# Optimization experiments

Hardware: AMD Instinct MI355X
Metric: run time of the kernel (lower is better)

Reference implementation:

```python
import jax, jax.numpy as jnp
import numpy as np
import math

K, D_FEAT, L_FACT, N = 128, 512, 64, 4096


def setup_inputs() -> dict:
    key = jax.random.key(0)
    k1, k2, k3, k4 = jax.random.split(key, 4)
    x = jax.random.normal(k1, (N, D_FEAT), dtype=jnp.float32)
    MU = jax.random.normal(k2, (K, D_FEAT), dtype=jnp.float32)
    A = jax.random.normal(k3, (K, D_FEAT, L_FACT), dtype=jnp.float32) * 0.1
    D = jax.random.uniform(k4, (K, D_FEAT), dtype=jnp.float32, minval=0.5, maxval=1.5)
    PI = jnp.ones((K,), dtype=jnp.float32) / K
    return {"x": x, "MU": MU, "A": A, "D": D, "PI": PI}


def reference(x, MU, A, D, PI):
    # Woodbury-identity MFA log-likelihood: Sigma_k = A_k A_k^T + diag(D_k^2)
    Kc, d, l = A.shape
    iD = D ** -2.0                                    # (K, d)  inverse diagonal noise
    AiD = A * iD[:, :, None]                          # (K, d, l) = diag(iD) @ A
    # L_k = I_l + A_k^T diag(iD_k) A_k   (small l x l capacitance matrix)
    Lmat = jnp.eye(l, dtype=x.dtype)[None] + jnp.einsum('kdl,kdm->klm', A, AiD)
    iL = jnp.linalg.inv(Lmat)                         # (K, l, l)
    # q1[k,n] = sum_d iD[k,d] * (x[n,d] - MU[k,d])^2, expanded to avoid (K,N,d)
    q1 = ((x ** 2) @ iD.T                             # (N, K)
          - 2.0 * (x @ (iD * MU).T)
          + jnp.sum(iD * MU ** 2, axis=1)[None, :]).T  # (K, N)
    # t[k,n,:] = (diag(iD_k) A_k)^T (x_n - MU_k)
    t = jnp.einsum('nd,kdl->knl', x, AiD) - jnp.einsum('kd,kdl->kl', MU, AiD)[:, None, :]
    # q2[k,n] = t^T iL_k t  (Woodbury correction quadratic form)
    q2 = jnp.einsum('knl,klm,knm->kn', t, iL, t)      # (K, N)
    m_d = q1 - q2                                     # Mahalanobis distances (K, N)
    log_det_L = jnp.linalg.slogdet(Lmat)[1]           # L is PD -> log(det(L))
    log_det_Sigma = log_det_L - jnp.sum(jnp.log(iD), axis=1)
    const = d * math.log(2.0 * math.pi)
    # NOTE: original code adds PI (not log PI) -- kept faithful.
    per_comp = PI[:, None] - 0.5 * ((const + log_det_Sigma)[:, None] + m_d)  # (K, N)
    return jax.scipy.special.logsumexp(per_comp, axis=0)  # (N,)
```

## Files before the change

kernel.cpp:

```cpp
#include <hip/hip_runtime.h>
#include <math.h>


#define KC 128
#define DF 512
#define LF 64
#define NN 4096

typedef __attribute__((ext_vector_type(8))) short short8;
typedef __attribute__((ext_vector_type(4))) float f32x4;

static __device__ __forceinline__ unsigned short bfr(float f) {
  union { float f; unsigned u; } v; v.f = f;
  return (unsigned short)((v.u + 0x7FFFu + ((v.u >> 16) & 1u)) >> 16);
}
static __device__ __forceinline__ float b2f(unsigned short u) {
  union { unsigned u; float f; } v; v.u = ((unsigned)u) << 16; return v.f;
}
static __device__ __forceinline__ void ldst16(void* lds, const void* g) {
  __builtin_amdgcn_global_load_lds((const __attribute__((address_space(1))) void*)g,
                                   (__attribute__((address_space(3))) void*)lds,
                                   16, 0, 0);
}

__global__ __launch_bounds__(256) void mfa_prep(const float* __restrict__ x,
                                                const float* __restrict__ A,
                                                const float* __restrict__ Dp,
                                                unsigned short* __restrict__ xaug,
                                                unsigned short* __restrict__ As,
                                                unsigned short* __restrict__ Ast) {
  int b = blockIdx.x, tid = threadIdx.x;
  if (b < 1024) {
    int k = b >> 3, dc = b & 7;
    __shared__ float siDs[64];
    __shared__ unsigned short Tr[64][72];
    if (tid < 64) siDs[tid] = 1.0f / Dp[k * DF + dc * 64 + tid];
    __syncthreads();
#pragma unroll
    for (int q = 0; q < 4; ++q) {
      int f = q * 256 + tid;
      int dd = f >> 4, i4 = (f & 15) * 4;
      float4 v = *reinterpret_cast<const float4*>(&A[((size_t)(k * DF + dc * 64 + dd)) * LF + i4]);
      float s = siDs[dd];
      ushort4 u;
      u.x = bfr(v.x * s); u.y = bfr(v.y * s); u.z = bfr(v.z * s); u.w = bfr(v.w * s);
      *reinterpret_cast<ushort4*>(&As[((size_t)(k * DF + dc * 64 + dd)) * LF + i4]) = u;
      *reinterpret_cast<ushort4*>(&Tr[dd][i4]) = u;
    }
    __syncthreads();
    int i = tid >> 2, ds0 = (tid & 3) * 16;
    unsigned short t16[16];
#pragma unroll
    for (int e = 0; e < 16; ++e) t16[e] = Tr[ds0 + e][i];
    uint4 v0, v1;
    v0.x = (unsigned)t16[0] | ((unsigned)t16[1] << 16);
    v0.y = (unsigned)t16[2] | ((unsigned)t16[3] << 16);
    v0.z = (unsigned)t16[4] | ((unsigned)t16[5] << 16);
    v0.w = (unsigned)t16[6] | ((unsigned)t16[7] << 16);
    v1.x = (unsigned)t16[8] | ((unsigned)t16[9] << 16);
    v1.y = (unsigned)t16[10] | ((unsigned)t16[11] << 16);
    v1.z = (unsigned)t16[12] | ((unsigned)t16[13] << 16);
    v1.w = (unsigned)t16[14] | ((unsigned)t16[15] << 16);
    size_t ro = ((size_t)(k * LF + i)) * DF + dc * 64 + ds0;
    *reinterpret_cast<uint4*>(&Ast[ro]) = v0;
    *reinterpret_cast<uint4*>(&Ast[ro + 8]) = v1;
  } else {
    int f = (b - 1024) * 256 + tid;
    float4 v = reinterpret_cast<const float4*>(x)[f];
    int n = f >> 7, c4 = (f & 127) << 2;
    ushort4 a, s;
    a.x = bfr(v.x); a.y = bfr(v.y); a.z = bfr(v.z); a.w = bfr(v.w);
    s.x = bfr(v.x * v.x); s.y = bfr(v.y * v.y); s.z = bfr(v.z * v.z); s.w = bfr(v.w * v.w);
    *reinterpret_cast<ushort4*>(&xaug[(size_t)n * 1024 + c4]) = a;
    *reinterpret_cast<ushort4*>(&xaug[(size_t)n * 1024 + 512 + c4]) = s;
  }
}

__global__ __launch_bounds__(256) void mfa_percomp(const float* __restrict__ MU,
                                                   const float* __restrict__ Dp,
                                                   const float* __restrict__ PI,
                                                   const unsigned short* __restrict__ Ast,
                                                   const unsigned short* __restrict__ As,
                                                   unsigned short* __restrict__ Waug,
                                                   unsigned short* __restrict__ Gt,
                                                   float* __restrict__ hws,
                                                   float* __restrict__ c0g) {
  int k = blockIdx.x, tid = threadIdx.x, lane = tid & 63, w = tid >> 6;
  __shared__ float S[64 * 132];
  __shared__ unsigned short Tile[64 * 64];
  __shared__ float smuS[DF];
  __shared__ float m2part[256];
  __shared__ float m2S[64];
  __shared__ float invd_s[64];
  __shared__ float redq[80];
  __shared__ float c0a_s;

  for (int idx = tid; idx < 4096; idx += 256) {
    int r = idx >> 6, c = idx & 63;
    S[r * 132 + 64 + c] = (r == c) ? 1.f : 0.f;
  }

  {
    float slog = 0.f, smu2 = 0.f;
#pragma unroll
    for (int p = 0; p < 2; ++p) {
      int d = p * 256 + tid;
      float Dv = Dp[k * DF + d];
      float id = 1.f / (Dv * Dv);
      float mu = MU[k * DF + d];
      float wv = id * mu;
      smuS[d] = mu / Dv;
      Waug[(size_t)k * 1024 + d] = bfr(wv);
      Waug[(size_t)k * 1024 + 512 + d] = bfr(-0.5f * id);
      slog += logf(id);
      smu2 += wv * mu;
    }
#pragma unroll
    for (int m = 1; m < 64; m <<= 1) {
      slog += __shfl_xor(slog, m, 64);
      smu2 += __shfl_xor(smu2, m, 64);
    }
    if (lane == 0) { redq[w] = slog; redq[8 + w] = smu2; }
  }
  __syncthreads();
  if (tid == 0) {
    float sl = 0.f, sm = 0.f;
    for (int q = 0; q < 4; ++q) { sl += redq[q]; sm += redq[8 + q]; }
    c0a_s = PI[k] - 0.5f * (DF * 1.8378770664093453f + sm - sl);
  }

  f32x4 accL[4];
  f32x4 zero = {0.f, 0.f, 0.f, 0.f};
#pragma unroll
  for (int nj = 0; nj < 4; ++nj) accL[nj] = zero;
  int lr = lane >> 3, lc = lane & 7;
  int gcs = (lc ^ lr) * 8;
  float m2acc = 0.f;
  int mi_i = tid & 63, mi_g = tid >> 6;
  for (int kt = 0; kt < 8; ++kt) {
#pragma unroll
    for (int it = 0; it < 2; ++it) {
      int row = w * 8 + it * 32 + lr;
      ldst16(&Tile[(w * 8 + it * 32) * 64], Ast + ((size_t)(k * LF + row)) * DF + kt * 64 + gcs);
    }
    __syncthreads();
#pragma unroll
    for (int kk = 0; kk < 2; ++kk) {
      int sw = ((kk * 4 + (lane >> 4)) ^ (lane & 7)) * 8;
      short8 av = *reinterpret_cast<const short8*>(&Tile[(w * 16 + (lane & 15)) * 64 + sw]);
#pragma unroll
      for (int nj = 0; nj < 4; ++nj) {
        short8 bv = *reinterpret_cast<const short8*>(&Tile[(nj * 16 + (lane & 15)) * 64 + sw]);
        accL[nj] = __builtin_amdgcn_mfma_f32_16x16x32_bf16(av, bv, accL[nj], 0, 0, 0);
      }
    }
#pragma unroll
    for (int c2 = 0; c2 < 2; ++c2) {
      int g = mi_g * 2 + c2;
      int slot = g ^ (mi_i & 7);
      const unsigned* cp = reinterpret_cast<const unsigned*>(&Tile[mi_i * 64 + slot * 8]);
#pragma unroll
      for (int u2 = 0; u2 < 4; ++u2) {
        unsigned uu = cp[u2];
        int d0 = kt * 64 + g * 8 + u2 * 2;
        m2acc += b2f((unsigned short)(uu & 0xFFFF)) * smuS[d0];
        m2acc += b2f((unsigned short)(uu >> 16)) * smuS[d0 + 1];
      }
    }
    __syncthreads();
  }
#pragma unroll
  for (int nj = 0; nj < 4; ++nj)
#pragma unroll
    for (int reg = 0; reg < 4; ++reg) {
      int m = w * 16 + (lane >> 4) * 4 + reg;
      int n = nj * 16 + (lane & 15);
      S[m * 132 + n] = accL[nj][reg] + (m == n ? 1.f : 0.f);
    }
  m2part[tid] = m2acc;
  __syncthreads();
  if (tid < 64) m2S[tid] = m2part[tid] + m2part[tid + 64] + m2part[tid + 128] + m2part[tid + 192];

  {
    int rg = tid >> 4, cg = tid & 15;
    for (int Jo = 0; Jo < 16; ++Jo) {
      int J = Jo * 4;
      __syncthreads();
      f32x4 B0 = *reinterpret_cast<f32x4*>(&S[(J + 0) * 132 + J]);
      f32x4 B1 = *reinterpret_cast<f32x4*>(&S[(J + 1) * 132 + J]);
      f32x4 B2 = *reinterpret_cast<f32x4*>(&S[(J + 2) * 132 + J]);
      f32x4 B3 = *reinterpret_cast<f32x4*>(&S[(J + 3) * 132 + J]);
      int cc = J + 4 + cg * 4;
      f32x4 S0 = *reinterpret_cast<f32x4*>(&S[(J + 0) * 132 + cc]);
      f32x4 S1 = *reinterpret_cast<f32x4*>(&S[(J + 1) * 132 + cc]);
      f32x4 S2 = *reinterpret_cast<f32x4*>(&S[(J + 2) * 132 + cc]);
      f32x4 S3 = *reinterpret_cast<f32x4*>(&S[(J + 3) * 132 + cc]);
      f32x4 V[4], TGT[4];
#pragma unroll
      for (int a = 0; a < 4; ++a) {
        int r = J + rg + 16 * a;
        if (r < 64) {
          V[a] = *reinterpret_cast<f32x4*>(&S[r * 132 + J]);
          TGT[a] = *reinterpret_cast<f32x4*>(&S[r * 132 + cc]);
        }
      }
      __syncthreads();
      float p0 = 1.0f / B0[0];
      float m10 = B1[0] * p0;  B1 -= m10 * B0;
      float m20 = B2[0] * p0;  B2 -= m20 * B0;
      float m30 = B3[0] * p0;  B3 -= m30 * B0;
      float p1 = 1.0f / B1[1];
      float m21 = B2[1] * p1;  B2 -= m21 * B1;
      float m31 = B3[1] * p1;  B3 -= m31 * B1;
      float p2 = 1.0f / B2[2];
      float m32 = B3[2] * p2;  B3 -= m32 * B2;
      float p3 = 1.0f / B3[3];
      float T1_0 = -m10;
      float T2_1 = -m21, T2_0 = -m20 - m21 * T1_0;
      float T3_2 = -m32, T3_1 = -m31 - m32 * T2_1, T3_0 = -m30 - m31 * T1_0 - m32 * T2_0;
      if (cg == 0 && rg < 4) {
        f32x4 bw = (rg == 0) ? B0 : (rg == 1) ? B1 : (rg == 2) ? B2 : B3;
        *reinterpret_cast<f32x4*>(&S[(J + rg) * 132 + J]) = bw;
      }
#pragma unroll
      for (int a = 0; a < 4; ++a) {
        int r = J + rg + 16 * a;
        if (r < 64) {
          f32x4 v = V[a];
          float n0 = v[0] * p0;
          float t1 = v[1] - n0 * B0[1];
          float n1 = t1 * p1;
          float t2 = v[2] - n0 * B0[2] - n1 * B1[2];
          float n2 = t2 * p2;
          float t3 = v[3] - n0 * B0[3] - n1 * B1[3] - n2 * B2[3];
          float n3 = t3 * p3;
          int pi = r - J;
          if (pi < 1) n0 = 0.f;
          if (pi < 2) n1 = 0.f;
          if (pi < 3) n2 = 0.f;
          if (pi < 4) n3 = 0.f;
          float cA = n0 + n1 * T1_0 + n2 * T2_0 + n3 * T3_0;
          float cB = n1 + n2 * T2_1 + n3 * T3_1;
          float cC = n2 + n3 * T3_2;
          float cD = n3;
          f32x4 res = TGT[a] - cA * S0 - cB * S1 - cC * S2 - cD * S3;
          *reinterpret_cast<f32x4*>(&S[r * 132 + cc]) = res;
        }
      }
    }
  }
  __syncthreads();
  if (tid < 64) {
    float dg2 = S[tid * 132 + tid];
    invd_s[tid] = rsqrtf(dg2);
    redq[tid] = logf(dg2);
  }
  __syncthreads();
  if (tid == 0) {
    float s = 0.f;
    for (int q = 0; q < 64; ++q) s += redq[q];
    c0g[k] = c0a_s - 0.5f * s;
  }
  if (tid < 64) {
    float hsum = 0.f;
#pragma unroll
    for (int j2 = 0; j2 < 64; ++j2) hsum += S[tid * 132 + 64 + j2] * m2S[j2];
    hws[k * 64 + tid] = hsum * invd_s[tid];
  }
  unsigned short* Wbs = Tile;
  {
    int l = tid >> 2;
#pragma unroll
    for (int q = 0; q < 2; ++q) {
      int sc = (tid & 3) * 2 + q;
      int gch = sc ^ (l & 7);
      float il = invd_s[l];
      unsigned short t8[8];
#pragma unroll
      for (int e = 0; e < 8; ++e) t8[e] = bfr(il * S[l * 132 + 64 + gch * 8 + e]);
      uint4 val;
      val.x = (unsigned)t8[0] | ((unsigned)t8[1] << 16);
      val.y = (unsigned)t8[2] | ((unsigned)t8[3] << 16);
      val.z = (unsigned)t8[4] | ((unsigned)t8[5] << 16);
      val.w = (unsigned)t8[6] | ((unsigned)t8[7] << 16);
      *reinterpret_cast<uint4*>(&Wbs[l * 64 + sc * 8]) = val;
    }
  }
  __syncthreads();
  unsigned short* DsA = reinterpret_cast<unsigned short*>(S);
  unsigned short* CoutA = reinterpret_cast<unsigned short*>(S) + 8192;
  for (int dq = 0; dq < 4; ++dq) {
#pragma unroll
    for (int it = 0; it < 4; ++it) {
      int row = w * 8 + it * 32 + lr;
      ldst16(&DsA[(w * 8 + it * 32) * 64], As + ((size_t)(k * DF + dq * 128 + row)) * LF + gcs);
    }
    __syncthreads();
    f32x4 gacc[4][2];
#pragma unroll
    for (int mi = 0; mi < 4; ++mi)
#pragma unroll
      for (int nj = 0; nj < 2; ++nj) gacc[mi][nj] = zero;
#pragma unroll
    for (int kk = 0; kk < 2; ++kk) {
      int sw = ((kk * 4 + (lane >> 4)) ^ (lane & 7)) * 8;
      short8 av[4], bv[2];
#pragma unroll
      for (int mi = 0; mi < 4; ++mi)
        av[mi] = *reinterpret_cast<const short8*>(&Wbs[(mi * 16 + (lane & 15)) * 64 + sw]);
#pragma unroll
      for (int nj = 0; nj < 2; ++nj)
        bv[nj] = *reinterpret_cast<const short8*>(&DsA[(w * 32 + nj * 16 + (lane & 15)) * 64 + sw]);
#pragma unroll
      for (int mi = 0; mi < 4; ++mi)
#pragma unroll
        for (int nj = 0; nj < 2; ++nj)
          gacc[mi][nj] = __builtin_amdgcn_mfma_f32_16x16x32_bf16(av[mi], bv[nj], gacc[mi][nj], 0, 0, 0);
    }
    float siD[2];
#pragma unroll
    for (int nj = 0; nj < 2; ++nj)
      siD[nj] = 1.0f / Dp[k * DF + dq * 128 + w * 32 + nj * 16 + (lane & 15)];
#pragma unroll
    for (int mi = 0; mi < 4; ++mi)
#pragma unroll
      for (int nj = 0; nj < 2; ++nj) {
        int dl = w * 32 + nj * 16 + (lane & 15);
#pragma unroll
        for (int reg = 0; reg < 4; ++reg) {
          int l = mi * 16 + (lane >> 4) * 4 + reg;
          CoutA[l * 132 + dl] = bfr(gacc[mi][nj][reg] * siD[nj]);
        }
      }
    __syncthreads();
    {
      int l = tid >> 2, seg = (tid & 3) * 32;
      uint4* dst = reinterpret_cast<uint4*>(&Gt[((size_t)(k * LF + l)) * DF + dq * 128 + seg]);
#pragma unroll
      for (int u = 0; u < 4; ++u) {
        unsigned short t8[8];
#pragma unroll
        for (int e = 0; e < 8; ++e) t8[e] = CoutA[l * 132 + seg + u * 8 + e];
        uint4 val;
        val.x = (unsigned)t8[0] | ((unsigned)t8[1] << 16);
        val.y = (unsigned)t8[2] | ((unsigned)t8[3] << 16);
        val.z = (unsigned)t8[4] | ((unsigned)t8[5] << 16);
        val.w = (unsigned)t8[6] | ((unsigned)t8[7] << 16);
        dst[u] = val;
      }
    }
    __syncthreads();
  }
}

__global__ __launch_bounds__(256) void mfa_q1g(const unsigned short* __restrict__ xaug,
                                               const unsigned short* __restrict__ Waug,
                                               float* __restrict__ r12p) {
  int nb = blockIdx.x * 128, kq = blockIdx.y;
  int tid = threadIdx.x, lane = tid & 63, w = tid >> 6, wx = w & 1, wy = w >> 1;
  __shared__ unsigned short As[128 * 64];
  __shared__ unsigned short Bs[128 * 64];
  f32x4 acc[4][4];
  f32x4 zero = {0.f, 0.f, 0.f, 0.f};
#pragma unroll
  for (int mi = 0; mi < 4; ++mi)
#pragma unroll
    for (int nj = 0; nj < 4; ++nj) acc[mi][nj] = zero;
  const unsigned short* xg = xaug + (size_t)nb * 1024;
  int lr = lane >> 3, lc = lane & 7;
  int gcs = (lc ^ lr) * 8;
  for (int kt = 0; kt < 4; ++kt) {
    int kof = kq * 256 + kt * 64;
#pragma unroll
    for (int it = 0; it < 4; ++it) {
      int row = w * 8 + it * 32 + lr;
      ldst16(&As[(w * 8 + it * 32) * 64], xg + (size_t)row * 1024 + kof + gcs);
      ldst16(&Bs[(w * 8 + it * 32) * 64], Waug + (size_t)row * 1024 + kof + gcs);
    }
    __syncthreads();
#pragma unroll
    for (int kk = 0; kk < 2; ++kk) {
      int sw = ((kk * 4 + (lane >> 4)) ^ (lane & 7)) * 8;
      short8 av[4], bv[4];
#pragma unroll
      for (int mi = 0; mi < 4; ++mi)
        av[mi] = *reinterpret_cast<const short8*>(&As[(wy * 64 + mi * 16 + (lane & 15)) * 64 + sw]);
#pragma unroll
      for (int nj = 0; nj < 4; ++nj)
        bv[nj] = *reinterpret_cast<const short8*>(&Bs[(wx * 64 + nj * 16 + (lane & 15)) * 64 + sw]);
#pragma unroll
      for (int mi = 0; mi < 4; ++mi)
#pragma unroll
        for (int nj = 0; nj < 4; ++nj)
          acc[mi][nj] = __builtin_amdgcn_mfma_f32_16x16x32_bf16(av[mi], bv[nj], acc[mi][nj], 0, 0, 0);
    }
    __syncthreads();
  }
  float* outp = r12p + (size_t)kq * KC * NN;
#pragma unroll
  for (int mi = 0; mi < 4; ++mi)
#pragma unroll
    for (int nj = 0; nj < 4; ++nj) {
      int ccol = wx * 64 + nj * 16 + (lane & 15);
      int nrow = nb + wy * 64 + mi * 16 + (lane >> 4) * 4;
      float4 o;
      o.x = acc[mi][nj][0]; o.y = acc[mi][nj][1]; o.z = acc[mi][nj][2]; o.w = acc[mi][nj][3];
      *reinterpret_cast<float4*>(&outp[(size_t)ccol * NN + nrow]) = o;
    }
}

__global__ __launch_bounds__(256) void mfa_main(const unsigned short* __restrict__ xaug,
                                                const unsigned short* __restrict__ Gt,
                                                const float* __restrict__ hws,
                                                const float* __restrict__ c0g,
                                                const float* __restrict__ r12p,
                                                float* __restrict__ s2b) {
  int bx = blockIdx.x, by = blockIdx.y;
  int tid = threadIdx.x, lane = tid & 63, w = tid >> 6, wx = w & 1, wy = w >> 1;
  __shared__ unsigned short As[128 * 64];
  __shared__ unsigned short Bs[128 * 64];
  f32x4 acc[4][4];
  f32x4 zero = {0.f, 0.f, 0.f, 0.f};
#pragma unroll
  for (int mi = 0; mi < 4; ++mi)
#pragma unroll
    for (int nj = 0; nj < 4; ++nj) acc[mi][nj] = zero;
  int nbase = by * 128, cbase = bx * 128;
  const unsigned short* xg = xaug + (size_t)nbase * 1024;
  const unsigned short* gg = Gt + (size_t)cbase * DF;
  int lr = lane >> 3, lc = lane & 7;
  int gcs = (lc ^ lr) * 8;
  for (int kt = 0; kt < 8; ++kt) {
#pragma unroll
    for (int it = 0; it < 4; ++it) {
      int row = w * 8 + it * 32 + lr;
      ldst16(&As[(w * 8 + it * 32) * 64], xg + (size_t)row * 1024 + kt * 64 + gcs);
      ldst16(&Bs[(w * 8 + it * 32) * 64], gg + (size_t)row * DF + kt * 64 + gcs);
    }
    __syncthreads();
#pragma unroll
    for (int kk = 0; kk < 2; ++kk) {
      int sw = ((kk * 4 + (lane >> 4)) ^ (lane & 7)) * 8;
      short8 av[4], bv[4];
#pragma unroll
      for (int mi = 0; mi < 4; ++mi)
        av[mi] = *reinterpret_cast<const short8*>(&As[(wy * 64 + mi * 16 + (lane & 15)) * 64 + sw]);
#pragma unroll
      for (int nj = 0; nj < 4; ++nj)
        bv[nj] = *reinterpret_cast<const short8*>(&Bs[(wx * 64 + nj * 16 + (lane & 15)) * 64 + sw]);
#pragma unroll
      for (int mi = 0; mi < 4; ++mi)
#pragma unroll
        for (int nj = 0; nj < 4; ++nj)
          acc[mi][nj] = __builtin_amdgcn_mfma_f32_16x16x32_bf16(av[mi], bv[nj], acc[mi][nj], 0, 0, 0);
    }
    __syncthreads();
  }
  int comp = bx * 2 + wx;
  float hv[4];
#pragma unroll
  for (int nj = 0; nj < 4; ++nj) hv[nj] = hws[comp * 64 + nj * 16 + (lane & 15)];
  float cc = c0g[comp];
  int rbase = nbase + wy * 64;
#pragma unroll
  for (int mi = 0; mi < 4; ++mi) {
    f32x4 sv;
#pragma unroll
    for (int reg = 0; reg < 4; ++reg) {
      float s = 0.f;
#pragma unroll
      for (int nj = 0; nj < 4; ++nj) {
        float dlt = acc[mi][nj][reg] - hv[nj];
        s += dlt * dlt;
      }
      s += __shfl_xor(s, 1, 64);
      s += __shfl_xor(s, 2, 64);
      s += __shfl_xor(s, 4, 64);
      s += __shfl_xor(s, 8, 64);
      sv[reg] = s;
    }
    if ((lane & 15) == 0) {
      int nr = rbase + mi * 16 + (lane >> 4) * 4;
      size_t idx = (size_t)comp * NN + nr;
      float4 r0 = *reinterpret_cast<const float4*>(&r12p[idx]);
      float4 r1 = *reinterpret_cast<const float4*>(&r12p[(size_t)KC * NN + idx]);
      float4 r2 = *reinterpret_cast<const float4*>(&r12p[(size_t)2 * KC * NN + idx]);
      float4 r3 = *reinterpret_cast<const float4*>(&r12p[(size_t)3 * KC * NN + idx]);
      float4 o;
      o.x = 0.5f * sv[0] + cc + r0.x + r1.x + r2.x + r3.x;
      o.y = 0.5f * sv[1] + cc + r0.y + r1.y + r2.y + r3.y;
      o.z = 0.5f * sv[2] + cc + r0.z + r1.z + r2.z + r3.z;
      o.w = 0.5f * sv[3] + cc + r0.w + r1.w + r2.w + r3.w;
      *reinterpret_cast<float4*>(&s2b[idx]) = o;
    }
  }
}

__global__ __launch_bounds__(64) void mfa_lse(const float* __restrict__ s2b,
                                              float* __restrict__ out) {
  int n = blockIdx.x * 64 + threadIdx.x;
  float m = -3.0e38f, s = 0.f;
#pragma unroll 8
  for (int k = 0; k < KC; ++k) {
    float t = s2b[(size_t)k * NN + n];
    float nm = fmaxf(m, t);
    s = s * expf(m - nm) + expf(t - nm);
    m = nm;
  }
  out[n] = m + logf(s);
}

extern "C" void kernel_launch(void* const* d_in, const int* in_sizes, int n_in,
                              void* d_out, int out_size, void* d_ws, size_t ws_size,
                              hipStream_t stream) {
  const float* x  = (const float*)d_in[0];
  const float* MU = (const float*)d_in[1];
  const float* A  = (const float*)d_in[2];
  const float* Dp = (const float*)d_in[3];
  const float* PI = (const float*)d_in[4];
  float* out = (float*)d_out;

  char* base = (char*)d_ws;
  size_t off = 0;
  auto alloc = [&](size_t bytes) -> void* {
    void* p = base + off;
    off += (bytes + 255) & ~(size_t)255;
    return p;
  };
  unsigned short* xaug = (unsigned short*)alloc((size_t)NN * 1024 * 2);
  unsigned short* As   = (unsigned short*)alloc((size_t)KC * DF * LF * 2);
  unsigned short* Ast  = (unsigned short*)alloc((size_t)KC * LF * DF * 2);
  unsigned short* Waug = (unsigned short*)alloc((size_t)KC * 1024 * 2);
  unsigned short* Gt   = (unsigned short*)alloc((size_t)KC * LF * DF * 2);
  float* hws           = (float*)alloc((size_t)KC * 64 * 4);
  float* c0g           = (float*)alloc((size_t)KC * 4);
  float* r12p          = (float*)alloc((size_t)4 * KC * NN * 4);
  float* s2b           = (float*)alloc((size_t)KC * NN * 4);

  mfa_prep<<<3072, 256, 0, stream>>>(x, A, Dp, xaug, As, Ast);
  mfa_percomp<<<KC, 256, 0, stream>>>(MU, Dp, PI, Ast, As, Waug, Gt, hws, c0g);
  mfa_q1g<<<dim3(NN / 128, 4), 256, 0, stream>>>(xaug, Waug, r12p);
  mfa_main<<<dim3(64, NN / 128), 256, 0, stream>>>(xaug, Gt, hws, c0g, r12p, s2b);
  mfa_lse<<<NN / 64, 64, 0, stream>>>(s2b, out);
}
```

Before: 168.7 us.

## Fuse q1 GEMM into main kernel as extra heavy block column; batch percomp tile loads

Removes the separate mfa_q1g launch. mfa_main gets one extra block column (bx==0) that computes the full q1 GEMM over K=1024 against Waug and writes a single r12 buffer, which mfa_lse then adds. This replaces the four split-K partial buffers that mfa_main used to read. Separately, mfa_percomp now loads four Ast k-tiles per sync into the S shared buffer, cutting the number of barriers, and moves the identity initialisation to after the loop. The heavy column does twice the K-loop work of the other columns, which risks load imbalance and a long tail.

New measurement: 186.4 us. +10.5%, slower.

```diff
diff --git a/kernel.cpp b/kernel.cpp
--- a/kernel.cpp
+++ b/kernel.cpp
@@ -87,18 +87,14 @@
                                                    float* __restrict__ c0g) {
   int k = blockIdx.x, tid = threadIdx.x, lane = tid & 63, w = tid >> 6;
   __shared__ float S[64 * 132];
-  __shared__ unsigned short Tile[64 * 64];
+  __shared__ unsigned short Wbs[64 * 64];
   __shared__ float smuS[DF];
   __shared__ float m2part[256];
   __shared__ float m2S[64];
   __shared__ float invd_s[64];
   __shared__ float redq[80];
   __shared__ float c0a_s;
-
-  for (int idx = tid; idx < 4096; idx += 256) {
-    int r = idx >> 6, c = idx & 63;
-    S[r * 132 + 64 + c] = (r == c) ? 1.f : 0.f;
-  }
+  unsigned short* Tile = reinterpret_cast<unsigned short*>(S);
 
   {
     float slog = 0.f, smu2 = 0.f;
@@ -137,37 +133,50 @@
   int gcs = (lc ^ lr) * 8;
   float m2acc = 0.f;
   int mi_i = tid & 63, mi_g = tid >> 6;
-  for (int kt = 0; kt < 8; ++kt) {
-#pragma unroll
-    for (int it = 0; it < 2; ++it) {
-      int row = w * 8 + it * 32 + lr;
-      ldst16(&Tile[(w * 8 + it * 32) * 64], Ast + ((size_t)(k * LF + row)) * DF + kt * 64 + gcs);
-    }
-    __syncthreads();
-#pragma unroll
-    for (int kk = 0; kk < 2; ++kk) {
-      int sw = ((kk * 4 + (lane >> 4)) ^ (lane & 7)) * 8;
-      short8 av = *reinterpret_cast<const short8*>(&Tile[(w * 16 + (lane & 15)) * 64 + sw]);
-#pragma unroll
-      for (int nj = 0; nj < 4; ++nj) {
-        short8 bv = *reinterpret_cast<const short8*>(&Tile[(nj * 16 + (lane & 15)) * 64 + sw]);
-        accL[nj] = __builtin_amdgcn_mfma_f32_16x16x32_bf16(av, bv, accL[nj], 0, 0, 0);
-      }
-    }
-#pragma unroll
-    for (int c2 = 0; c2 < 2; ++c2) {
-      int g = mi_g * 2 + c2;
-      int slot = g ^ (mi_i & 7);
-      const unsigned* cp = reinterpret_cast<const unsigned*>(&Tile[mi_i * 64 + slot * 8]);
-#pragma unroll
-      for (int u2 = 0; u2 < 4; ++u2) {
-        unsigned uu = cp[u2];
-        int d0 = kt * 64 + g * 8 + u2 * 2;
-        m2acc += b2f((unsigned short)(uu & 0xFFFF)) * smuS[d0];
-        m2acc += b2f((unsigned short)(uu >> 16)) * smuS[d0 + 1];
-      }
-    }
-    __syncthreads();
+  for (int half = 0; half < 2; ++half) {
+    __syncthreads();
+#pragma unroll
+    for (int kt2 = 0; kt2 < 4; ++kt2) {
+      int kt = half * 4 + kt2;
+#pragma unroll
+      for (int it = 0; it < 2; ++it) {
+        int row = w * 8 + it * 32 + lr;
+        ldst16(&Tile[(kt2 * 64 + w * 8 + it * 32) * 64],
+               Ast + ((size_t)(k * LF + row)) * DF + kt * 64 + gcs);
+      }
+    }
+    __syncthreads();
+#pragma unroll
+    for (int kt2 = 0; kt2 < 4; ++kt2) {
+#pragma unroll
+      for (int kk = 0; kk < 2; ++kk) {
+        int sw = ((kk * 4 + (lane >> 4)) ^ (lane & 7)) * 8;
+        short8 av = *reinterpret_cast<const short8*>(&Tile[(kt2 * 64 + w * 16 + (lane & 15)) * 64 + sw]);
+#pragma unroll
+        for (int nj = 0; nj < 4; ++nj) {
+          short8 bv = *reinterpret_cast<const short8*>(&Tile[(kt2 * 64 + nj * 16 + (lane & 15)) * 64 + sw]);
+          accL[nj] = __builtin_amdgcn_mfma_f32_16x16x32_bf16(av, bv, accL[nj], 0, 0, 0);
+        }
+      }
+#pragma unroll
+      for (int c2 = 0; c2 < 2; ++c2) {
+        int g = mi_g * 2 + c2;
+        int slot = g ^ (mi_i & 7);
+        const unsigned* cp = reinterpret_cast<const unsigned*>(&Tile[(kt2 * 64 + mi_i) * 64 + slot * 8]);
+#pragma unroll
+        for (int u2 = 0; u2 < 4; ++u2) {
+          unsigned uu = cp[u2];
+          int d0 = (half * 4 + kt2) * 64 + g * 8 + u2 * 2;
+          m2acc += b2f((unsigned short)(uu & 0xFFFF)) * smuS[d0];
+          m2acc += b2f((unsigned short)(uu >> 16)) * smuS[d0 + 1];
+        }
+      }
+    }
+  }
+  __syncthreads();
+  for (int idx = tid; idx < 4096; idx += 256) {
+    int r = idx >> 6, c = idx & 63;
+    S[r * 132 + 64 + c] = (r == c) ? 1.f : 0.f;
   }
 #pragma unroll
   for (int nj = 0; nj < 4; ++nj)
@@ -267,7 +276,6 @@
     for (int j2 = 0; j2 < 64; ++j2) hsum += S[tid * 132 + 64 + j2] * m2S[j2];
     hws[k * 64 + tid] = hsum * invd_s[tid];
   }
-  unsigned short* Wbs = Tile;
   {
     int l = tid >> 2;
 #pragma unroll
@@ -289,6 +297,7 @@
   __syncthreads();
   unsigned short* DsA = reinterpret_cast<unsigned short*>(S);
   unsigned short* CoutA = reinterpret_cast<unsigned short*>(S) + 8192;
+  f32x4 zero2 = {0.f, 0.f, 0.f, 0.f};
   for (int dq = 0; dq < 4; ++dq) {
 #pragma unroll
     for (int it = 0; it < 4; ++it) {
@@ -300,7 +309,7 @@
 #pragma unroll
     for (int mi = 0; mi < 4; ++mi)
 #pragma unroll
-      for (int nj = 0; nj < 2; ++nj) gacc[mi][nj] = zero;
+      for (int nj = 0; nj < 2; ++nj) gacc[mi][nj] = zero2;
 #pragma unroll
     for (int kk = 0; kk < 2; ++kk) {
       int sw = ((kk * 4 + (lane >> 4)) ^ (lane & 7)) * 8;
@@ -353,67 +362,12 @@
   }
 }
 
-__global__ __launch_bounds__(256) void mfa_q1g(const unsigned short* __restrict__ xaug,
-                                               const unsigned short* __restrict__ Waug,
-                                               float* __restrict__ r12p) {
-  int nb = blockIdx.x * 128, kq = blockIdx.y;
-  int tid = threadIdx.x, lane = tid & 63, w = tid >> 6, wx = w & 1, wy = w >> 1;
-  __shared__ unsigned short As[128 * 64];
-  __shared__ unsigned short Bs[128 * 64];
-  f32x4 acc[4][4];
-  f32x4 zero = {0.f, 0.f, 0.f, 0.f};
-#pragma unroll
-  for (int mi = 0; mi < 4; ++mi)
-#pragma unroll
-    for (int nj = 0; nj < 4; ++nj) acc[mi][nj] = zero;
-  const unsigned short* xg = xaug + (size_t)nb * 1024;
-  int lr = lane >> 3, lc = lane & 7;
-  int gcs = (lc ^ lr) * 8;
-  for (int kt = 0; kt < 4; ++kt) {
-    int kof = kq * 256 + kt * 64;
-#pragma unroll
-    for (int it = 0; it < 4; ++it) {
-      int row = w * 8 + it * 32 + lr;
-      ldst16(&As[(w * 8 + it * 32) * 64], xg + (size_t)row * 1024 + kof + gcs);
-      ldst16(&Bs[(w * 8 + it * 32) * 64], Waug + (size_t)row * 1024 + kof + gcs);
-    }
-    __syncthreads();
-#pragma unroll
-    for (int kk = 0; kk < 2; ++kk) {
-      int sw = ((kk * 4 + (lane >> 4)) ^ (lane & 7)) * 8;
-      short8 av[4], bv[4];
-#pragma unroll
-      for (int mi = 0; mi < 4; ++mi)
-        av[mi] = *reinterpret_cast<const short8*>(&As[(wy * 64 + mi * 16 + (lane & 15)) * 64 + sw]);
-#pragma unroll
-      for (int nj = 0; nj < 4; ++nj)
-        bv[nj] = *reinterpret_cast<const short8*>(&Bs[(wx * 64 + nj * 16 + (lane & 15)) * 64 + sw]);
-#pragma unroll
-      for (int mi = 0; mi < 4; ++mi)
-#pragma unroll
-        for (int nj = 0; nj < 4; ++nj)
-          acc[mi][nj] = __builtin_amdgcn_mfma_f32_16x16x32_bf16(av[mi], bv[nj], acc[mi][nj], 0, 0, 0);
-    }
-    __syncthreads();
-  }
-  float* outp = r12p + (size_t)kq * KC * NN;
-#pragma unroll
-  for (int mi = 0; mi < 4; ++mi)
-#pragma unroll
-    for (int nj = 0; nj < 4; ++nj) {
-      int ccol = wx * 64 + nj * 16 + (lane & 15);
-      int nrow = nb + wy * 64 + mi * 16 + (lane >> 4) * 4;
-      float4 o;
-      o.x = acc[mi][nj][0]; o.y = acc[mi][nj][1]; o.z = acc[mi][nj][2]; o.w = acc[mi][nj][3];
-      *reinterpret_cast<float4*>(&outp[(size_t)ccol * NN + nrow]) = o;
-    }
-}
-
 __global__ __launch_bounds__(256) void mfa_main(const unsigned short* __restrict__ xaug,
                                                 const unsigned short* __restrict__ Gt,
+                                                const unsigned short* __restrict__ Waug,
                                                 const float* __restrict__ hws,
                                                 const float* __restrict__ c0g,
-                                                const float* __restrict__ r12p,
+                                                float* __restrict__ r12,
                                                 float* __restrict__ s2b) {
   int bx = blockIdx.x, by = blockIdx.y;
   int tid = threadIdx.x, lane = tid & 63, w = tid >> 6, wx = w & 1, wy = w >> 1;
@@ -425,17 +379,22 @@
   for (int mi = 0; mi < 4; ++mi)
 #pragma unroll
     for (int nj = 0; nj < 4; ++nj) acc[mi][nj] = zero;
-  int nbase = by * 128, cbase = bx * 128;
+  bool heavy = (bx == 0);
+  int nkt = heavy ? 16 : 8;
+  int nbase = by * 128;
   const unsigned short* xg = xaug + (size_t)nbase * 1024;
-  const unsigned short* gg = Gt + (size_t)cbase * DF;
+  const unsigned short* gg;
+  size_t bstride;
+  if (heavy) { gg = Waug; bstride = 1024; }
+  else       { gg = Gt + (size_t)((bx - 1) * 128) * DF; bstride = DF; }
   int lr = lane >> 3, lc = lane & 7;
   int gcs = (lc ^ lr) * 8;
-  for (int kt = 0; kt < 8; ++kt) {
+  for (int kt = 0; kt < nkt; ++kt) {
 #pragma unroll
     for (int it = 0; it < 4; ++it) {
       int row = w * 8 + it * 32 + lr;
       ldst16(&As[(w * 8 + it * 32) * 64], xg + (size_t)row * 1024 + kt * 64 + gcs);
-      ldst16(&Bs[(w * 8 + it * 32) * 64], gg + (size_t)row * DF + kt * 64 + gcs);
+      ldst16(&Bs[(w * 8 + it * 32) * 64], gg + (size_t)row * bstride + kt * 64 + gcs);
     }
     __syncthreads();
 #pragma unroll
@@ -456,53 +415,63 @@
     }
     __syncthreads();
   }
-  int comp = bx * 2 + wx;
-  float hv[4];
-#pragma unroll
-  for (int nj = 0; nj < 4; ++nj) hv[nj] = hws[comp * 64 + nj * 16 + (lane & 15)];
-  float cc = c0g[comp];
-  int rbase = nbase + wy * 64;
-#pragma unroll
-  for (int mi = 0; mi < 4; ++mi) {
-    f32x4 sv;
-#pragma unroll
-    for (int reg = 0; reg < 4; ++reg) {
-      float s = 0.f;
+  if (heavy) {
+#pragma unroll
+    for (int mi = 0; mi < 4; ++mi)
 #pragma unroll
       for (int nj = 0; nj < 4; ++nj) {
-        float dlt = acc[mi][nj][reg] - hv[nj];
-        s += dlt * dlt;
-      }
-      s += __shfl_xor(s, 1, 64);
-      s += __shfl_xor(s, 2, 64);
-      s += __shfl_xor(s, 4, 64);
-      s += __shfl_xor(s, 8, 64);
-      sv[reg] = s;
-    }
-    if ((lane & 15) == 0) {
-      int nr = rbase + mi * 16 + (lane >> 4) * 4;
-      size_t idx = (size_t)comp * NN + nr;
-      float4 r0 = *reinterpret_cast<const float4*>(&r12p[idx]);
-      float4 r1 = *reinterpret_cast<const float4*>(&r12p[(size_t)KC * NN + idx]);
-      float4 r2 = *reinterpret_cast<const float4*>(&r12p[(size_t)2 * KC * NN + idx]);
-      float4 r3 = *reinterpret_cast<const float4*>(&r12p[(size_t)3 * KC * NN + idx]);
-      float4 o;
-      o.x = 0.5f * sv[0] + cc + r0.x + r1.x + r2.x + r3.x;
-      o.y = 0.5f * sv[1] + cc + r0.y + r1.y + r2.y + r3.y;
-      o.z = 0.5f * sv[2] + cc + r0.z + r1.z + r2.z + r3.z;
-      o.w = 0.5f * sv[3] + cc + r0.w + r1.w + r2.w + r3.w;
-      *reinterpret_cast<float4*>(&s2b[idx]) = o;
+        int ccol = wx * 64 + nj * 16 + (lane & 15);
+        int nrow = nbase + wy * 64 + mi * 16 + (lane >> 4) * 4;
+        float4 o;
+        o.x = acc[mi][nj][0]; o.y = acc[mi][nj][1]; o.z = acc[mi][nj][2]; o.w = acc[mi][nj][3];
+        *reinterpret_cast<float4*>(&r12[(size_t)ccol * NN + nrow]) = o;
+      }
+  } else {
+    int comp = (bx - 1) * 2 + wx;
+    float hv[4];
+#pragma unroll
+    for (int nj = 0; nj < 4; ++nj) hv[nj] = hws[comp * 64 + nj * 16 + (lane & 15)];
+    float cc = c0g[comp];
+    int rbase = nbase + wy * 64;
+#pragma unroll
+    for (int mi = 0; mi < 4; ++mi) {
+      f32x4 sv;
+#pragma unroll
+      for (int reg = 0; reg < 4; ++reg) {
+        float s = 0.f;
+#pragma unroll
+        for (int nj = 0; nj < 4; ++nj) {
+          float dlt = acc[mi][nj][reg] - hv[nj];
+          s += dlt * dlt;
+        }
+        s += __shfl_xor(s, 1, 64);
+        s += __shfl_xor(s, 2, 64);
+        s += __shfl_xor(s, 4, 64);
+        s += __shfl_xor(s, 8, 64);
+        sv[reg] = s;
+      }
+      if ((lane & 15) == 0) {
+        int nr = rbase + mi * 16 + (lane >> 4) * 4;
+        size_t idx = (size_t)comp * NN + nr;
+        float4 o;
+        o.x = 0.5f * sv[0] + cc;
+        o.y = 0.5f * sv[1] + cc;
+        o.z = 0.5f * sv[2] + cc;
+        o.w = 0.5f * sv[3] + cc;
+        *reinterpret_cast<float4*>(&s2b[idx]) = o;
+      }
     }
   }
 }
 
 __global__ __launch_bounds__(64) void mfa_lse(const float* __restrict__ s2b,
+                                              const float* __restrict__ r12,
                                               float* __restrict__ out) {
   int n = blockIdx.x * 64 + threadIdx.x;
   float m = -3.0e38f, s = 0.f;
 #pragma unroll 8
   for (int k = 0; k < KC; ++k) {
-    float t = s2b[(size_t)k * NN + n];
+    float t = s2b[(size_t)k * NN + n] + r12[(size_t)k * NN + n];
     float nm = fmaxf(m, t);
     s = s * expf(m - nm) + expf(t - nm);
     m = nm;
@@ -534,12 +503,11 @@
   unsigned short* Gt   = (unsigned short*)alloc((size_t)KC * LF * DF * 2);
   float* hws           = (float*)alloc((size_t)KC * 64 * 4);
   float* c0g           = (float*)alloc((size_t)KC * 4);
-  float* r12p          = (float*)alloc((size_t)4 * KC * NN * 4);
+  float* r12           = (float*)alloc((size_t)KC * NN * 4);
   float* s2b           = (float*)alloc((size_t)KC * NN * 4);
 
   mfa_prep<<<3072, 256, 0, stream>>>(x, A, Dp, xaug, As, Ast);
   mfa_percomp<<<KC, 256, 0, stream>>>(MU, Dp, PI, Ast, As, Waug, Gt, hws, c0g);
-  mfa_q1g<<<dim3(NN / 128, 4), 256, 0, stream>>>(xaug, Waug, r12p);
-  mfa_main<<<dim3(64, NN / 128), 256, 0, stream>>>(xaug, Gt, hws, c0g, r12p, s2b);
-  mfa_lse<<<NN / 64, 64, 0, stream>>>(s2b, out);
-}
+  mfa_main<<<dim3(65, NN / 128), 256, 0, stream>>>(xaug, Gt, Waug, hws, c0g, r12, s2b);
+  mfa_lse<<<NN / 64, 64, 0, stream>>>(s2b, r12, out);
+}
```
